# Performance work log

Measured on AMD Instinct MI355X. Metric: run time of the kernel, lower is better.

Reference implementation:

```python
import jax, jax.numpy as jnp
import numpy as np

N = 8192        # num nodes
E = 262144      # num edges (avg degree 32)
IN_DIM = 256
OUT_DIM = 256
NEG_SLOPE = 0.2


def setup_inputs() -> dict:
    key = jax.random.key(0)
    k1, k2, k3, k4 = jax.random.split(key, 4)
    x = jax.random.normal(k1, (N, IN_DIM), dtype=jnp.float32)
    edge_index = jax.random.randint(k2, (2, E), 0, N, dtype=jnp.int64)
    # learned params: W of Linear(in_dim,out_dim,bias=False) stored as (in_dim,out_dim),
    # attn Linear(2*out_dim,1,bias=False) stored as flat vector a of shape (2*out_dim,)
    W = jax.random.normal(k3, (IN_DIM, OUT_DIM), dtype=jnp.float32) * (1.0 / np.sqrt(IN_DIM))
    a = jax.random.normal(k4, (2 * OUT_DIM,), dtype=jnp.float32) * (1.0 / np.sqrt(2 * OUT_DIM))
    return {"x": x, "edge_index": edge_index, "W": W, "a": a}


def reference(x, edge_index, W, a):
    # h = W(x): (N, out_dim)
    h = x @ W
    src, tgt = edge_index[0], edge_index[1]
    # attn(cat(h[src], h[tgt])) == h[src] @ a_src + h[tgt] @ a_tgt
    a_src, a_tgt = a[:OUT_DIM], a[OUT_DIM:]
    e = jax.nn.leaky_relu(h[src] @ a_src + h[tgt] @ a_tgt, negative_slope=NEG_SLOPE)  # (E,)
    # faithful to original: scatter scores into dense (N,N) zeros, dense softmax over rows
    alpha = jnp.zeros((N, N), dtype=x.dtype).at[src, tgt].set(e)
    alpha = jax.nn.softmax(alpha, axis=-1)
    # dropout is identity in eval / p=0
    out = alpha @ h  # (N, out_dim)
    return out
```

## Files before the change

kernel.cpp:

```cpp
#include <hip/hip_runtime.h>
#include <math.h>

#define N_NODES 8192
#define E_EDGES 262144
#define DIM 256
#define NEG_SLOPE 0.2f
#define ROW_CAP 128

typedef __attribute__((ext_vector_type(8))) short short8;
typedef __attribute__((ext_vector_type(4))) float f32x4;

#define OFF_HB       0u
#define OFF_XB       4194304u
#define OFF_WT       8388608u
#define OFF_CURSOR   8519680u
#define OFF_SV       8552448u
#define OFF_TV       8585216u
#define OFF_SALL     8617984u
#define ZERO_BASE    OFF_CURSOR
#define ZERO_BYTES   99328u
#define ZERO_VEC4    6208u
#define OFF_CSR      8620032u

__device__ __forceinline__ unsigned f2bf(float f) {
  unsigned u = __float_as_uint(f);
  u += 0x7fffu + ((u >> 16) & 1u);
  return u >> 16;
}

__global__ __launch_bounds__(256) void setup_kernel(const float* __restrict__ x,
                                                    const float* __restrict__ W,
                                                    unsigned short* __restrict__ xb,
                                                    unsigned short* __restrict__ wt,
                                                    float4* __restrict__ zero_p) {
  const int b = blockIdx.x;
  const int t = threadIdx.x;
  if (b < 1024) {
    const int i = b * 2048 + t * 8;
    const float4 v0 = *(const float4*)(x + i);
    const float4 v1 = *(const float4*)(x + i + 4);
    uint4 o;
    o.x = f2bf(v0.x) | (f2bf(v0.y) << 16);
    o.y = f2bf(v0.z) | (f2bf(v0.w) << 16);
    o.z = f2bf(v1.x) | (f2bf(v1.y) << 16);
    o.w = f2bf(v1.z) | (f2bf(v1.w) << 16);
    *(uint4*)(xb + i) = o;
  } else if (b < 1088) {
    const int idx = (b - 1024) * 1024 + t * 4;
    const int n = idx >> 8;
    const int k = idx & 255;
    uint2 o;
    o.x = f2bf(W[(size_t)k * DIM + n]) | (f2bf(W[(size_t)(k + 1) * DIM + n]) << 16);
    o.y = f2bf(W[(size_t)(k + 2) * DIM + n]) | (f2bf(W[(size_t)(k + 3) * DIM + n]) << 16);
    *(uint2*)(wt + idx) = o;
  } else {
    const unsigned i = (b - 1088) * 256 + t;
    if (i < ZERO_VEC4) zero_p[i] = float4{0.f, 0.f, 0.f, 0.f};
  }
}

__global__ __launch_bounds__(256) void gemm_scatter_kernel(const unsigned short* __restrict__ xb,
                                                           const unsigned short* __restrict__ wt,
                                                           const float* __restrict__ a,
                                                           unsigned short* __restrict__ hb,
                                                           float* __restrict__ sv,
                                                           float* __restrict__ tv,
                                                           float* __restrict__ S_all,
                                                           const int* __restrict__ ei,
                                                           int* __restrict__ cursor,
                                                           int* __restrict__ csr) {
  const int bid = blockIdx.x;
  if (bid >= 256) {
    const int k0e = (bid - 256) * 256 + threadIdx.x;
#pragma unroll
    for (int h = 0; h < 2; ++h) {
      const int k = k0e + h * 131072;
      const int src = ei[k];
      const int tgt = ei[E_EDGES + k];
      const int pos = atomicAdd(&cursor[src], 1);
      if (pos < ROW_CAP) csr[src * ROW_CAP + pos] = tgt;
    }
    return;
  }
  __shared__ unsigned short Al[2][128 * 64];
  __shared__ unsigned short Bl[2][64 * 64];
  const int bx = bid >> 2, by = bid & 3;
  const int m0 = bx * 128, n0 = by * 64;
  const int t = threadIdx.x;
  const int w = t >> 6, l = t & 63;
  const int q = l >> 4, l15 = l & 15;

  f32x4 acc[2][4] = {{{0.f,0.f,0.f,0.f},{0.f,0.f,0.f,0.f},{0.f,0.f,0.f,0.f},{0.f,0.f,0.f,0.f}},
                     {{0.f,0.f,0.f,0.f},{0.f,0.f,0.f,0.f},{0.f,0.f,0.f,0.f},{0.f,0.f,0.f,0.f}}};

  const int lrow = l >> 3;
  const int kvs = (l & 7) ^ lrow;

  auto stage = [&](int ki, int buf) {
    const int k0 = ki * 64;
#pragma unroll
    for (int o = 0; o < 4; ++o) {
      const int op = w * 4 + o;
      const unsigned short* gp = xb + (size_t)(m0 + op * 8 + lrow) * DIM + k0 + kvs * 8;
      __builtin_amdgcn_global_load_lds((const __attribute__((address_space(1))) unsigned*)gp,
                                       (__attribute__((address_space(3))) unsigned*)(&Al[buf][op * 512]),
                                       16, 0, 0);
    }
#pragma unroll
    for (int o = 0; o < 2; ++o) {
      const int op = w * 2 + o;
      const unsigned short* gp = wt + (size_t)(n0 + op * 8 + lrow) * DIM + k0 + kvs * 8;
      __builtin_amdgcn_global_load_lds((const __attribute__((address_space(1))) unsigned*)gp,
                                       (__attribute__((address_space(3))) unsigned*)(&Bl[buf][op * 512]),
                                       16, 0, 0);
    }
  };

  stage(0, 0);
  int buf = 0;
  for (int ki = 0; ki < 4; ++ki) {
    asm volatile("s_waitcnt vmcnt(0)" ::: "memory");
    __builtin_amdgcn_s_barrier();
    if (ki < 3) stage(ki + 1, buf ^ 1);
#pragma unroll
    for (int s = 0; s < 2; ++s) {
      const int kv = s * 4 + q;
      short8 af[2], bf[4];
#pragma unroll
      for (int mi = 0; mi < 2; ++mi) {
        const int m = w * 32 + mi * 16 + l15;
        af[mi] = *(const short8*)(&Al[buf][m * 64 + ((kv ^ (m & 7)) * 8)]);
      }
#pragma unroll
      for (int nt = 0; nt < 4; ++nt) {
        const int n = nt * 16 + l15;
        bf[nt] = *(const short8*)(&Bl[buf][n * 64 + ((kv ^ (n & 7)) * 8)]);
      }
#pragma unroll
      for (int mi = 0; mi < 2; ++mi)
#pragma unroll
        for (int nt = 0; nt < 4; ++nt)
          acc[mi][nt] = __builtin_amdgcn_mfma_f32_16x16x32_bf16(af[mi], bf[nt], acc[mi][nt], 0, 0, 0);
    }
    buf ^= 1;
  }

  float asv[4], atv[4];
#pragma unroll
  for (int nt = 0; nt < 4; ++nt) {
    const int n = n0 + nt * 16 + l15;
    asv[nt] = a[n];
    atv[nt] = a[DIM + n];
  }
#pragma unroll
  for (int mi = 0; mi < 2; ++mi)
#pragma unroll
    for (int r = 0; r < 4; ++r) {
      float sp = 0.f, tp = 0.f;
#pragma unroll
      for (int nt = 0; nt < 4; ++nt) {
        const float v = acc[mi][nt][r];
        sp += v * asv[nt];
        tp += v * atv[nt];
      }
#pragma unroll
      for (int off = 1; off < 16; off <<= 1) {
        sp += __shfl_xor(sp, off);
        tp += __shfl_xor(tp, off);
      }
      if (l15 == 0) {
        const int m = m0 + w * 32 + mi * 16 + q * 4 + r;
        atomicAdd(&sv[m], sp);
        atomicAdd(&tv[m], tp);
      }
    }
#pragma unroll
  for (int nt = 0; nt < 4; ++nt) {
    float cs = 0.f;
#pragma unroll
    for (int mi = 0; mi < 2; ++mi)
#pragma unroll
      for (int r = 0; r < 4; ++r) cs += acc[mi][nt][r];
    cs += __shfl_xor(cs, 16);
    cs += __shfl_xor(cs, 32);
    if (q == 0) atomicAdd(&S_all[n0 + nt * 16 + l15], cs);
  }
#pragma unroll
  for (int mi = 0; mi < 2; ++mi)
#pragma unroll
    for (int r = 0; r < 4; ++r) {
      const int m = m0 + w * 32 + mi * 16 + q * 4 + r;
#pragma unroll
      for (int nt = 0; nt < 4; ++nt)
        hb[(size_t)m * DIM + n0 + nt * 16 + l15] = (unsigned short)f2bf(acc[mi][nt][r]);
    }
}

__global__ __launch_bounds__(256) void row_kernel(const unsigned short* __restrict__ hb,
                                                  const float* __restrict__ sv,
                                                  const float* __restrict__ tv,
                                                  const float* __restrict__ S_all,
                                                  const int* __restrict__ cursor,
                                                  const int* __restrict__ csr,
                                                  float* __restrict__ out) {
  __shared__ unsigned bm[4][256];
  const int w = threadIdx.x >> 6;
  const int lane = threadIdx.x & 63;
  const int row = blockIdx.x * 4 + w;
#pragma unroll
  for (int i = lane; i < 256; i += 64) bm[w][i] = 0u;

  const int n_total = min(cursor[row], ROW_CAP);
  const float srow = sv[row];

  float4 acc = {0.f, 0.f, 0.f, 0.f};
  float zacc = 0.f;

  for (int e0 = 0; e0 < n_total; e0 += 64) {
    const int cn = min(64, n_total - e0);
    float wgt = 0.f;
    int tg = 0;
    if (lane < cn) {
      tg = csr[row * ROW_CAP + e0 + lane];
      const unsigned msk = 1u << (tg & 31);
      const unsigned old = atomicOr(&bm[w][tg >> 5], msk);
      if (!(old & msk)) {
        float ev = srow + tv[tg];
        ev = (ev > 0.f) ? ev : NEG_SLOPE * ev;
        wgt = expm1f(ev);
      }
    }
    zacc += wgt;
    for (int j = 0; j < cn; j += 8) {
#pragma unroll
      for (int u = 0; u < 8; ++u) {
        const int tj = __builtin_amdgcn_readlane(tg, j + u);
        const float wj = __uint_as_float(
            (unsigned)__builtin_amdgcn_readlane((int)__float_as_uint(wgt), j + u));
        const uint2 p = *(const uint2*)(hb + (size_t)tj * DIM + (lane << 2));
        acc.x += wj * __uint_as_float(p.x << 16);
        acc.y += wj * __uint_as_float(p.x & 0xffff0000u);
        acc.z += wj * __uint_as_float(p.y << 16);
        acc.w += wj * __uint_as_float(p.y & 0xffff0000u);
      }
    }
  }

#pragma unroll
  for (int off = 1; off < 64; off <<= 1) zacc += __shfl_xor(zacc, off);

  const float4 sa = *(const float4*)(S_all + (lane << 2));
  const float inv = 1.0f / ((float)N_NODES + zacc);
  float4 o;
  o.x = (sa.x + acc.x) * inv;
  o.y = (sa.y + acc.y) * inv;
  o.z = (sa.z + acc.z) * inv;
  o.w = (sa.w + acc.w) * inv;
  *(float4*)(out + (size_t)row * DIM + (lane << 2)) = o;
}

extern "C" void kernel_launch(void* const* d_in, const int* in_sizes, int n_in,
                              void* d_out, int out_size, void* d_ws, size_t ws_size,
                              hipStream_t stream) {
  const float* x = (const float*)d_in[0];
  const int* ei = (const int*)d_in[1];
  const float* W = (const float*)d_in[2];
  const float* a = (const float*)d_in[3];
  float* out = (float*)d_out;

  unsigned char* ws = (unsigned char*)d_ws;
  unsigned short* hb = (unsigned short*)(ws + OFF_HB);
  unsigned short* xb = (unsigned short*)(ws + OFF_XB);
  unsigned short* wt = (unsigned short*)(ws + OFF_WT);
  int* cursor = (int*)(ws + OFF_CURSOR);
  float* sv = (float*)(ws + OFF_SV);
  float* tv = (float*)(ws + OFF_TV);
  float* S_all = (float*)(ws + OFF_SALL);
  int* csr = (int*)(ws + OFF_CSR);

  setup_kernel<<<1113, 256, 0, stream>>>(x, W, xb, wt, (float4*)(ws + ZERO_BASE));
  gemm_scatter_kernel<<<768, 256, 0, stream>>>(xb, wt, a, hb, sv, tv, S_all, ei, cursor, csr);
  row_kernel<<<N_NODES / 4, 256, 0, stream>>>(hb, sv, tv, S_all, cursor, csr, out);
}
```

Measured before the change: 104.8 us.

## Fuse x fp32-to-bf16 conversion into GEMM A-operand register loads

Removes the separate pass that converts x to bf16 in the setup kernel. Instead, each GEMM wave loads its A rows directly from fp32 x into registers, converts them and keeps the whole 256-wide K slice as MFMA fragments, dropping the A tile from LDS. This avoids writing and rereading an 4MB bf16 copy of x. The cost is that each block reads fp32 x, twice the bytes, with uncoalesced per-lane loads, and register pressure rises from holding 16 short8 fragments.

```diff
diff --git a/kernel.cpp b/kernel.cpp
--- a/kernel.cpp
+++ b/kernel.cpp
@@ -28,25 +28,13 @@
   return u >> 16;
 }
 
-__global__ __launch_bounds__(256) void setup_kernel(const float* __restrict__ x,
-                                                    const float* __restrict__ W,
-                                                    unsigned short* __restrict__ xb,
+__global__ __launch_bounds__(256) void setup_kernel(const float* __restrict__ W,
                                                     unsigned short* __restrict__ wt,
                                                     float4* __restrict__ zero_p) {
   const int b = blockIdx.x;
   const int t = threadIdx.x;
-  if (b < 1024) {
-    const int i = b * 2048 + t * 8;
-    const float4 v0 = *(const float4*)(x + i);
-    const float4 v1 = *(const float4*)(x + i + 4);
-    uint4 o;
-    o.x = f2bf(v0.x) | (f2bf(v0.y) << 16);
-    o.y = f2bf(v0.z) | (f2bf(v0.w) << 16);
-    o.z = f2bf(v1.x) | (f2bf(v1.y) << 16);
-    o.w = f2bf(v1.z) | (f2bf(v1.w) << 16);
-    *(uint4*)(xb + i) = o;
-  } else if (b < 1088) {
-    const int idx = (b - 1024) * 1024 + t * 4;
+  if (b < 64) {
+    const int idx = b * 1024 + t * 4;
     const int n = idx >> 8;
     const int k = idx & 255;
     uint2 o;
@@ -54,12 +42,12 @@
     o.y = f2bf(W[(size_t)(k + 2) * DIM + n]) | (f2bf(W[(size_t)(k + 3) * DIM + n]) << 16);
     *(uint2*)(wt + idx) = o;
   } else {
-    const unsigned i = (b - 1088) * 256 + t;
+    const unsigned i = (b - 64) * 256 + t;
     if (i < ZERO_VEC4) zero_p[i] = float4{0.f, 0.f, 0.f, 0.f};
   }
 }
 
-__global__ __launch_bounds__(256) void gemm_scatter_kernel(const unsigned short* __restrict__ xb,
+__global__ __launch_bounds__(256) void gemm_scatter_kernel(const float* __restrict__ x,
                                                            const unsigned short* __restrict__ wt,
                                                            const float* __restrict__ a,
                                                            unsigned short* __restrict__ hb,
@@ -82,7 +70,6 @@
     }
     return;
   }
-  __shared__ unsigned short Al[2][128 * 64];
   __shared__ unsigned short Bl[2][64 * 64];
   const int bx = bid >> 2, by = bid & 3;
   const int m0 = bx * 128, n0 = by * 64;
@@ -90,22 +77,11 @@
   const int w = t >> 6, l = t & 63;
   const int q = l >> 4, l15 = l & 15;
 
-  f32x4 acc[2][4] = {{{0.f,0.f,0.f,0.f},{0.f,0.f,0.f,0.f},{0.f,0.f,0.f,0.f},{0.f,0.f,0.f,0.f}},
-                     {{0.f,0.f,0.f,0.f},{0.f,0.f,0.f,0.f},{0.f,0.f,0.f,0.f},{0.f,0.f,0.f,0.f}}};
-
   const int lrow = l >> 3;
   const int kvs = (l & 7) ^ lrow;
 
-  auto stage = [&](int ki, int buf) {
+  auto stageB = [&](int ki, int buf) {
     const int k0 = ki * 64;
-#pragma unroll
-    for (int o = 0; o < 4; ++o) {
-      const int op = w * 4 + o;
-      const unsigned short* gp = xb + (size_t)(m0 + op * 8 + lrow) * DIM + k0 + kvs * 8;
-      __builtin_amdgcn_global_load_lds((const __attribute__((address_space(1))) unsigned*)gp,
-                                       (__attribute__((address_space(3))) unsigned*)(&Al[buf][op * 512]),
-                                       16, 0, 0);
-    }
 #pragma unroll
     for (int o = 0; o < 2; ++o) {
       const int op = w * 2 + o;
@@ -116,21 +92,37 @@
     }
   };
 
-  stage(0, 0);
+  stageB(0, 0);
+
+  short8 afr[2][8];
+#pragma unroll
+  for (int mi = 0; mi < 2; ++mi) {
+    const float* rp = x + (size_t)(m0 + w * 32 + mi * 16 + l15) * DIM + q * 8;
+#pragma unroll
+    for (int ks = 0; ks < 8; ++ks) {
+      const float4 u0 = *(const float4*)(rp + ks * 32);
+      const float4 u1 = *(const float4*)(rp + ks * 32 + 4);
+      short8 f;
+      f[0] = (short)f2bf(u0.x); f[1] = (short)f2bf(u0.y);
+      f[2] = (short)f2bf(u0.z); f[3] = (short)f2bf(u0.w);
+      f[4] = (short)f2bf(u1.x); f[5] = (short)f2bf(u1.y);
+      f[6] = (short)f2bf(u1.z); f[7] = (short)f2bf(u1.w);
+      afr[mi][ks] = f;
+    }
+  }
+
+  f32x4 acc[2][4] = {{{0.f,0.f,0.f,0.f},{0.f,0.f,0.f,0.f},{0.f,0.f,0.f,0.f},{0.f,0.f,0.f,0.f}},
+                     {{0.f,0.f,0.f,0.f},{0.f,0.f,0.f,0.f},{0.f,0.f,0.f,0.f},{0.f,0.f,0.f,0.f}}};
+
   int buf = 0;
   for (int ki = 0; ki < 4; ++ki) {
     asm volatile("s_waitcnt vmcnt(0)" ::: "memory");
     __builtin_amdgcn_s_barrier();
-    if (ki < 3) stage(ki + 1, buf ^ 1);
+    if (ki < 3) stageB(ki + 1, buf ^ 1);
 #pragma unroll
     for (int s = 0; s < 2; ++s) {
       const int kv = s * 4 + q;
-      short8 af[2], bf[4];
-#pragma unroll
-      for (int mi = 0; mi < 2; ++mi) {
-        const int m = w * 32 + mi * 16 + l15;
-        af[mi] = *(const short8*)(&Al[buf][m * 64 + ((kv ^ (m & 7)) * 8)]);
-      }
+      short8 bf[4];
 #pragma unroll
       for (int nt = 0; nt < 4; ++nt) {
         const int n = nt * 16 + l15;
@@ -140,7 +132,8 @@
       for (int mi = 0; mi < 2; ++mi)
 #pragma unroll
         for (int nt = 0; nt < 4; ++nt)
-          acc[mi][nt] = __builtin_amdgcn_mfma_f32_16x16x32_bf16(af[mi], bf[nt], acc[mi][nt], 0, 0, 0);
+          acc[mi][nt] = __builtin_amdgcn_mfma_f32_16x16x32_bf16(afr[mi][ki * 2 + s], bf[nt],
+                                                                acc[mi][nt], 0, 0, 0);
     }
     buf ^= 1;
   }
@@ -270,7 +263,6 @@
 
   unsigned char* ws = (unsigned char*)d_ws;
   unsigned short* hb = (unsigned short*)(ws + OFF_HB);
-  unsigned short* xb = (unsigned short*)(ws + OFF_XB);
   unsigned short* wt = (unsigned short*)(ws + OFF_WT);
   int* cursor = (int*)(ws + OFF_CURSOR);
   float* sv = (float*)(ws + OFF_SV);
@@ -278,7 +270,7 @@
   float* S_all = (float*)(ws + OFF_SALL);
   int* csr = (int*)(ws + OFF_CSR);
 
-  setup_kernel<<<1113, 256, 0, stream>>>(x, W, xb, wt, (float4*)(ws + ZERO_BASE));
-  gemm_scatter_kernel<<<768, 256, 0, stream>>>(xb, wt, a, hb, sv, tv, S_all, ei, cursor, csr);
+  setup_kernel<<<89, 256, 0, stream>>>(W, wt, (float4*)(ws + ZERO_BASE));
+  gemm_scatter_kernel<<<768, 256, 0, stream>>>(x, wt, a, hb, sv, tv, S_all, ei, cursor, csr);
   row_kernel<<<N_NODES / 4, 256, 0, stream>>>(hb, sv, tv, S_all, cursor, csr, out);
 }
```

New measurement: 104.5 us. Within noise of the previous version (-0.3%).
